# Kernel tuning notes

Measured on AMD Instinct MI355X. Metric: run time of the kernel, lower is better.

## Reference

```python
import jax, jax.numpy as jnp
import numpy as np

B, C, H_IMG, W_LEN = 32, 32, 16, 512
IN_CH = C * H_IMG          # 512, LSTM input size
OUT_CH = 1024              # bidirectional output size
HID = OUT_CH // 2          # 512, hidden per direction


def setup_inputs() -> dict:
    key = jax.random.key(0)
    ks = jax.random.split(key, 9)
    s = 1.0 / np.sqrt(HID)  # torch LSTM default init scale
    u = lambda k, shape: jax.random.uniform(k, shape, jnp.float32, -s, s)
    return {
        "x": jax.random.normal(ks[0], (B, C, H_IMG, W_LEN), jnp.float32),
        "W_ih_f": u(ks[1], (4 * HID, IN_CH)),
        "W_hh_f": u(ks[2], (4 * HID, HID)),
        "b_ih_f": u(ks[3], (4 * HID,)),
        "b_hh_f": u(ks[4], (4 * HID,)),
        "W_ih_b": u(ks[5], (4 * HID, IN_CH)),
        "W_hh_b": u(ks[6], (4 * HID, HID)),
        "b_ih_b": u(ks[7], (4 * HID,)),
        "b_hh_b": u(ks[8], (4 * HID,)),
    }


def _lstm_dir(x, W_ih, W_hh, b_ih, b_hh, reverse):
    # x: [B, T, IN] -> h sequence [B, T, HID]; torch gate order (i, f, g, o)
    xp = jnp.einsum('bti,gi->btg', x, W_ih) + b_ih + b_hh  # input proj for all steps
    xp = jnp.swapaxes(xp, 0, 1)  # [T, B, 4H]
    if reverse:
        xp = xp[::-1]
    h0 = jnp.zeros((x.shape[0], HID), x.dtype)

    def step(carry, xp_t):
        h, c = carry
        g = xp_t + h @ W_hh.T
        i, f, gg, o = jnp.split(g, 4, axis=-1)
        c = jax.nn.sigmoid(f) * c + jax.nn.sigmoid(i) * jnp.tanh(gg)
        h = jax.nn.sigmoid(o) * jnp.tanh(c)
        return (h, c), h

    _, hs = jax.lax.scan(step, (h0, h0), xp)  # hs: [T, B, HID]
    if reverse:
        hs = hs[::-1]
    return jnp.swapaxes(hs, 0, 1)  # [B, T, HID]


def reference(x, W_ih_f, W_hh_f, b_ih_f, b_hh_f, W_ih_b, W_hh_b, b_ih_b, b_hh_b):
    Bn, Cn, Hn, Wn = x.shape
    # permute(0,3,1,2).view(B, W, C*H): width is the time axis
    xs = jnp.transpose(x, (0, 3, 1, 2)).reshape(Bn, Wn, Cn * Hn)
    hf = _lstm_dir(xs, W_ih_f, W_hh_f, b_ih_f, b_hh_f, reverse=False)
    hb = _lstm_dir(xs, W_ih_b, W_hh_b, b_ih_b, b_hh_b, reverse=True)
    out = jnp.concatenate([hf, hb], axis=-1)        # [B, W, OUT]
    out = jnp.swapaxes(out, 1, 2)                    # [B, OUT, W]
    return out.reshape(Bn, -1, Hn, Wn)               # [B, OUT//H, H, W]
```

## Files before the change

kernel.cpp:

```cpp
#include <hip/hip_runtime.h>
#include <hip/hip_bf16.h>

#define BATCH 32
#define TLEN 512
#define INCH 512
#define HID 512

typedef __bf16 bf16x8 __attribute__((ext_vector_type(8)));
typedef float f32x4 __attribute__((ext_vector_type(4)));
using bf16 = __hip_bfloat16;

#define OFF_XS2   0ull
#define OFF_WCAT  16777216ull
#define OFF_WHHP  20971520ull
#define OFF_BIAS  25165824ull
#define OFF_HBUF  25182208ull
#define OFF_CTR   25313280ull
#define OFF_FLAG  25313536ull
#define OFF_XP    25321728ull
#define WS_REQUIRED (25321728ull + 134217728ull)

__device__ __forceinline__ float sigmoid_fast(float x) {
    return 1.f / (1.f + __expf(-x));
}
__device__ __forceinline__ float tanh_fast(float x) {
    float ax = fabsf(x);
    float e = __expf(-2.f * ax);
    float r = (1.f - e) / (1.f + e);
    return copysignf(r, x);
}

__global__ void ws_too_small_kernel(float* out) {
    if (threadIdx.x == 0 && blockIdx.x == 0) out[0] = 12345.0f;
}

__global__ void pack_x_kernel(const float* __restrict__ x, bf16* __restrict__ XS2) {
    int bx = blockIdx.x;
    int b  = bx >> 6;
    int tt = (bx >> 3) & 7;
    int kt = bx & 7;
    __shared__ float tile[64][65];
    int tid  = threadIdx.x;
    int row2 = tid >> 6;
    int col  = tid & 63;
#pragma unroll
    for (int i = 0; i < 16; ++i) {
        int row = i * 4 + row2;
        int k = kt * 64 + row;
        tile[row][col] = x[((b * 32 + (k >> 4)) * 16 + (k & 15)) * 512 + tt * 64 + col];
    }
    __syncthreads();
#pragma unroll
    for (int i = 0; i < 16; ++i) {
        int trow = i * 4 + row2;
        int t = tt * 64 + trow;
        XS2[(t * 32 + b) * 512 + kt * 64 + col] = __float2bfloat16(tile[col][trow]);
    }
}

__global__ void pack_w_kernel(const float* __restrict__ Wih_f, const float* __restrict__ Whh_f,
                              const float* __restrict__ bih_f, const float* __restrict__ bhh_f,
                              const float* __restrict__ Wih_b, const float* __restrict__ Whh_b,
                              const float* __restrict__ bih_b, const float* __restrict__ bhh_b,
                              bf16* __restrict__ Wcat, bf16* __restrict__ Whhp,
                              float* __restrict__ bias, unsigned int* __restrict__ hbuf32,
                              unsigned int* __restrict__ ctr, unsigned int* __restrict__ flags) {
    long idx = (long)blockIdx.x * 256 + threadIdx.x;
    if (idx < 262144) {
        long e = idx * 8;
        int m = (int)(e >> 9), k = (int)(e & 511);
        const float* src = (m < 2048) ? &Wih_f[(long)m * 512 + k]
                                      : &Wih_b[(long)(m - 2048) * 512 + k];
        bf16* dst = &Wcat[e];
#pragma unroll
        for (int j = 0; j < 8; ++j) dst[j] = __float2bfloat16(src[j]);
        return;
    }
    idx -= 262144;
    if (idx < 262144) {
        long e = idx * 8;
        int k  = (int)(e & 511);
        int lm = (int)((e >> 9) & 63);
        int s  = (int)((e >> 15) & 31);
        int dir = (int)(e >> 20);
        int grow = (lm >> 4) * 512 + s * 16 + (lm & 15);
        const float* W = dir ? Whh_b : Whh_f;
        const float* src = &W[(long)grow * 512 + k];
        bf16* dst = &Whhp[e];
#pragma unroll
        for (int j = 0; j < 8; ++j) dst[j] = __float2bfloat16(src[j]);
        return;
    }
    idx -= 262144;
    if (idx < 4096) {
        int dir = (int)(idx >> 11), g = (int)(idx & 2047);
        bias[idx] = (dir ? (bih_b[g] + bhh_b[g]) : (bih_f[g] + bhh_f[g]));
        return;
    }
    idx -= 4096;
    if (idx < 32768) { hbuf32[idx] = 0u; return; }
    idx -= 32768;
    if (idx < 64) { ctr[idx] = 0u; return; }
    idx -= 64;
    if (idx < 2048) { flags[idx] = 0u; return; }
}

__global__ __launch_bounds__(256, 2) void gemm_xp_kernel(const bf16* __restrict__ Wcat,
                                                         const bf16* __restrict__ XS2,
                                                         bf16* __restrict__ XP) {
    int bm = (blockIdx.x & 31) * 128;
    int bn = (blockIdx.x >> 5) * 128;
    __shared__ bf16 lA[128 * 40];
    __shared__ bf16 lB[128 * 40];
    int tid = threadIdx.x;
    int lane = tid & 63, w = tid >> 6;
    int wm = (w & 1) * 64, wn = (w >> 1) * 64;
    int fr = lane & 15, fq = lane >> 4;
    f32x4 acc[4][4] = {};
    int r = tid >> 2, c = tid & 3;
    for (int kt = 0; kt < 16; ++kt) {
        int k0 = kt * 32;
        *(bf16x8*)&lA[r * 40 + c * 8]        = *(const bf16x8*)&Wcat[(long)(bm + r) * 512 + k0 + c * 8];
        *(bf16x8*)&lA[(r + 64) * 40 + c * 8] = *(const bf16x8*)&Wcat[(long)(bm + r + 64) * 512 + k0 + c * 8];
        *(bf16x8*)&lB[r * 40 + c * 8]        = *(const bf16x8*)&XS2[(long)(bn + r) * 512 + k0 + c * 8];
        *(bf16x8*)&lB[(r + 64) * 40 + c * 8] = *(const bf16x8*)&XS2[(long)(bn + r + 64) * 512 + k0 + c * 8];
        __syncthreads();
        bf16x8 af[4], bfm[4];
#pragma unroll
        for (int i = 0; i < 4; ++i) af[i]  = *(const bf16x8*)&lA[(wm + i * 16 + fr) * 40 + fq * 8];
#pragma unroll
        for (int i = 0; i < 4; ++i) bfm[i] = *(const bf16x8*)&lB[(wn + i * 16 + fr) * 40 + fq * 8];
#pragma unroll
        for (int mi = 0; mi < 4; ++mi)
#pragma unroll
            for (int ni = 0; ni < 4; ++ni)
                acc[mi][ni] = __builtin_amdgcn_mfma_f32_16x16x32_bf16(af[mi], bfm[ni], acc[mi][ni], 0, 0, 0);
        __syncthreads();
    }
#pragma unroll
    for (int mi = 0; mi < 4; ++mi) {
#pragma unroll
        for (int rr = 0; rr < 4; ++rr) {
            int m = bm + wm + mi * 16 + fq * 4 + rr;
            int dir = m >> 11, cc = m & 2047;
            int gate = cc >> 9, u = cc & 511, s = u >> 4, ul = u & 15;
#pragma unroll
            for (int ni = 0; ni < 4; ++ni) {
                int n = bn + wn + ni * 16 + fr;
                int t = n >> 5, b = n & 31;
                long off = ((((long)(t * 2 + dir) * 32 + s) * 4 + gate) * 16 + ul) * 32 + b;
                XP[off] = __float2bfloat16(acc[mi][ni][rr]);
            }
        }
    }
}

__global__ __launch_bounds__(512, 2) void lstm_rec_kernel(const bf16* __restrict__ Whhp,
                                                          const bf16* __restrict__ XP,
                                                          const float* __restrict__ bias,
                                                          bf16* hbuf, float* out,
                                                          unsigned int* flags) {
    int bx = blockIdx.x;
    int dir = bx >> 5, s = bx & 31;
    int tid = threadIdx.x;
    int lane = tid & 63, w = tid >> 6;
    int mt = w & 3, nt = w >> 2;
    int fr = lane & 15, fq = lane >> 4;
    __shared__ float gbuf[64 * 32];
    __shared__ float obuf[16][512];
    __shared__ bf16  hstage[BATCH * 16];
    __shared__ bf16  hsh[32 * 520];

    const bf16* wbase = Whhp + ((long)((dir * 32 + s) * 64 + mt * 16 + fr)) * 512 + fq * 8;
    bf16x8 wA[16];
#pragma unroll
    for (int kt = 0; kt < 16; ++kt) wA[kt] = *(const bf16x8*)(wbase + kt * 32);

    int b = tid & 31, ul = (tid >> 5) & 15;
    float bias_i = bias[dir * 2048 + 0 * 512 + s * 16 + ul];
    float bias_f = bias[dir * 2048 + 1 * 512 + s * 16 + ul];
    float bias_g = bias[dir * 2048 + 2 * 512 + s * 16 + ul];
    float bias_o = bias[dir * 2048 + 3 * 512 + s * 16 + ul];
    float cstate = 0.f;
    bf16* hb_dir = hbuf + (long)dir * 2 * BATCH * HID;
    unsigned int* myflag = flags + bx * 32;
    const unsigned int* pollflag = flags + (dir * 32 + (lane & 31)) * 32;
    long orow = (long)b * 524288 + (long)(dir * 512 + s * 16 + ul) * 512;
    int srow = tid >> 4, scol = (tid & 15) * 32;
    int guard_budget = 1 << 21;

    for (int t = 0; t < TLEN; ++t) {
        int ttime = dir ? (TLEN - 1 - t) : t;
        const bf16* xpp = XP + (long)(ttime * 2 + dir) * 65536 + (long)s * 2048;
        float xi = __bfloat162float(xpp[(0 * 16 + ul) * 32 + b]);
        float xf = __bfloat162float(xpp[(1 * 16 + ul) * 32 + b]);
        float xg = __bfloat162float(xpp[(2 * 16 + ul) * 32 + b]);
        float xo = __bfloat162float(xpp[(3 * 16 + ul) * 32 + b]);

        if (t > 0) {
            unsigned int target = (unsigned int)t;
            for (;;) {
                unsigned int v = __hip_atomic_load(pollflag, __ATOMIC_RELAXED,
                                                   __HIP_MEMORY_SCOPE_AGENT);
                if (__all(v >= target)) break;
                if (--guard_budget <= 0) break;
            }
        }

        {
            const bf16* src = hb_dir + (long)(t & 1) * BATCH * HID + (long)srow * 512 + scol;
            f32x4 v0, v1, v2, v3;
            asm volatile(
                "global_load_dwordx4 %0, %4, off sc0 sc1\n\t"
                "global_load_dwordx4 %1, %4, off offset:16 sc0 sc1\n\t"
                "global_load_dwordx4 %2, %4, off offset:32 sc0 sc1\n\t"
                "global_load_dwordx4 %3, %4, off offset:48 sc0 sc1\n\t"
                "s_waitcnt vmcnt(0)"
                : "=v"(v0), "=v"(v1), "=v"(v2), "=v"(v3)
                : "v"(src) : "memory");
            bf16* d = &hsh[srow * 520 + scol];
            *(f32x4*)(d)      = v0;
            *(f32x4*)(d + 8)  = v1;
            *(f32x4*)(d + 16) = v2;
            *(f32x4*)(d + 24) = v3;
        }
        __syncthreads();

        f32x4 acc = {};
#pragma unroll
        for (int kt = 0; kt < 16; ++kt) {
            bf16x8 hB = *(const bf16x8*)&hsh[(nt * 16 + fr) * 520 + kt * 32 + fq * 8];
            acc = __builtin_amdgcn_mfma_f32_16x16x32_bf16(wA[kt], hB, acc, 0, 0, 0);
        }
#pragma unroll
        for (int rr = 0; rr < 4; ++rr)
            gbuf[(mt * 16 + fq * 4 + rr) * 32 + nt * 16 + fr] = acc[rr];
        __syncthreads();

        float gi = xi + bias_i + gbuf[(0 * 16 + ul) * 32 + b];
        float gf = xf + bias_f + gbuf[(1 * 16 + ul) * 32 + b];
        float gg = xg + bias_g + gbuf[(2 * 16 + ul) * 32 + b];
        float go = xo + bias_o + gbuf[(3 * 16 + ul) * 32 + b];
        float si = sigmoid_fast(gi), sf = sigmoid_fast(gf), so = sigmoid_fast(go);
        cstate = sf * cstate + si * tanh_fast(gg);
        float h = so * tanh_fast(cstate);

        hstage[b * 16 + ul] = __float2bfloat16(h);
        obuf[ttime & 15][tid] = h;
        __syncthreads();

        if (w == 0) {
            int hbb = lane >> 1, half = lane & 1;
            f32x4 hv = *(const f32x4*)&hstage[hbb * 16 + half * 8];
            bf16* dst = hb_dir + (long)((t + 1) & 1) * BATCH * HID + (long)hbb * 512
                        + s * 16 + half * 8;
            asm volatile("global_store_dwordx4 %0, %1, off sc0 sc1"
                         :: "v"(dst), "v"(hv) : "memory");
            asm volatile("s_waitcnt vmcnt(0)" ::: "memory");
            if (lane == 0)
                __hip_atomic_store(myflag, (unsigned int)(t + 1), __ATOMIC_RELAXED,
                                   __HIP_MEMORY_SCOPE_AGENT);
        }

        if ((t & 15) == 15) {
            int tb = ttime & ~15;
            float vals[16];
#pragma unroll
            for (int c = 0; c < 16; ++c) vals[c] = obuf[c][tid];
            float* op = out + orow + tb;
#pragma unroll
            for (int c4 = 0; c4 < 4; ++c4)
                *(f32x4*)(op + c4 * 4) = *(f32x4*)&vals[c4 * 4];
        }
    }
}

extern "C" void kernel_launch(void* const* d_in, const int* in_sizes, int n_in,
                              void* d_out, int out_size, void* d_ws, size_t ws_size,
                              hipStream_t stream) {
    const float* x     = (const float*)d_in[0];
    const float* Wih_f = (const float*)d_in[1];
    const float* Whh_f = (const float*)d_in[2];
    const float* bih_f = (const float*)d_in[3];
    const float* bhh_f = (const float*)d_in[4];
    const float* Wih_b = (const float*)d_in[5];
    const float* Whh_b = (const float*)d_in[6];
    const float* bih_b = (const float*)d_in[7];
    const float* bhh_b = (const float*)d_in[8];
    float* out = (float*)d_out;

    if (ws_size < WS_REQUIRED) {
        ws_too_small_kernel<<<1, 64, 0, stream>>>(out);
        return;
    }

    char* ws = (char*)d_ws;
    bf16* XS2  = (bf16*)(ws + OFF_XS2);
    bf16* Wcat = (bf16*)(ws + OFF_WCAT);
    bf16* Whhp = (bf16*)(ws + OFF_WHHP);
    float* bias = (float*)(ws + OFF_BIAS);
    bf16* hbuf = (bf16*)(ws + OFF_HBUF);
    unsigned int* ctr   = (unsigned int*)(ws + OFF_CTR);
    unsigned int* flags = (unsigned int*)(ws + OFF_FLAG);
    bf16* XP   = (bf16*)(ws + OFF_XP);

    pack_x_kernel<<<2048, 256, 0, stream>>>(x, XS2);
    pack_w_kernel<<<2201, 256, 0, stream>>>(Wih_f, Whh_f, bih_f, bhh_f,
                                            Wih_b, Whh_b, bih_b, bhh_b,
                                            Wcat, Whhp, bias, (unsigned int*)hbuf, ctr, flags);
    gemm_xp_kernel<<<4096, 256, 0, stream>>>(Wcat, XS2, XP);
    lstm_rec_kernel<<<64, 512, 0, stream>>>(Whhp, XP, bias, hbuf, out, flags);
}
```

Measured before the change: 2.037 ms.

## Remove LDS barriers from LSTM recurrence via gate-interleaved weights and per-wave flags

Reorders the W_hh packing, the bias and the XP layout so each MFMA output lane holds all four gates (i,f,g,o) of one unit and batch element. The cell update can then run straight from accumulator registers, with no shared-memory gate buffer. Each wave loads h directly from global memory into MFMA B operands, stores its own h values, and raises its own per-wave flag. Pollers read four flags with one dwordx4 load. This removes all three __syncthreads and the LDS staging per timestep, at the cost of finer-grained flag traffic, scattered 2-byte global stores, and redundant global h loads across waves.

```diff
diff --git a/kernel.cpp b/kernel.cpp
--- a/kernel.cpp
+++ b/kernel.cpp
@@ -8,6 +8,8 @@
 
 typedef __bf16 bf16x8 __attribute__((ext_vector_type(8)));
 typedef float f32x4 __attribute__((ext_vector_type(4)));
+typedef unsigned int u32x4 __attribute__((ext_vector_type(4)));
+typedef unsigned short u16x4 __attribute__((ext_vector_type(4)));
 using bf16 = __hip_bfloat16;
 
 #define OFF_XS2   0ull
@@ -28,6 +30,10 @@
     float e = __expf(-2.f * ax);
     float r = (1.f - e) / (1.f + e);
     return copysignf(r, x);
+}
+__device__ __forceinline__ float bf2f(unsigned short u) {
+    unsigned int i = ((unsigned int)u) << 16;
+    float f; __builtin_memcpy(&f, &i, 4); return f;
 }
 
 __global__ void ws_too_small_kernel(float* out) {
@@ -83,7 +89,7 @@
         int lm = (int)((e >> 9) & 63);
         int s  = (int)((e >> 15) & 31);
         int dir = (int)(e >> 20);
-        int grow = (lm >> 4) * 512 + s * 16 + (lm & 15);
+        int grow = (lm & 3) * 512 + s * 16 + (lm >> 2);
         const float* W = dir ? Whh_b : Whh_f;
         const float* src = &W[(long)grow * 512 + k];
         bf16* dst = &Whhp[e];
@@ -93,7 +99,10 @@
     }
     idx -= 262144;
     if (idx < 4096) {
-        int dir = (int)(idx >> 11), g = (int)(idx & 2047);
+        int dir  = (int)(idx >> 11);
+        int r    = (int)(idx & 2047);
+        int s    = r >> 6, ul = (r >> 2) & 15, gate = r & 3;
+        int g    = gate * 512 + s * 16 + ul;
         bias[idx] = (dir ? (bih_b[g] + bhh_b[g]) : (bih_f[g] + bhh_f[g]));
         return;
     }
@@ -148,7 +157,7 @@
             for (int ni = 0; ni < 4; ++ni) {
                 int n = bn + wn + ni * 16 + fr;
                 int t = n >> 5, b = n & 31;
-                long off = ((((long)(t * 2 + dir) * 32 + s) * 4 + gate) * 16 + ul) * 32 + b;
+                long off = ((long)(t * 2 + dir) * 32 + s) * 2048 + (long)(ul * 32 + b) * 4 + gate;
                 XP[off] = __float2bfloat16(acc[mi][ni][rr]);
             }
         }
@@ -166,108 +175,106 @@
     int lane = tid & 63, w = tid >> 6;
     int mt = w & 3, nt = w >> 2;
     int fr = lane & 15, fq = lane >> 4;
-    __shared__ float gbuf[64 * 32];
     __shared__ float obuf[16][512];
-    __shared__ bf16  hstage[BATCH * 16];
-    __shared__ bf16  hsh[32 * 520];
 
     const bf16* wbase = Whhp + ((long)((dir * 32 + s) * 64 + mt * 16 + fr)) * 512 + fq * 8;
     bf16x8 wA[16];
 #pragma unroll
     for (int kt = 0; kt < 16; ++kt) wA[kt] = *(const bf16x8*)(wbase + kt * 32);
 
-    int b = tid & 31, ul = (tid >> 5) & 15;
-    float bias_i = bias[dir * 2048 + 0 * 512 + s * 16 + ul];
-    float bias_f = bias[dir * 2048 + 1 * 512 + s * 16 + ul];
-    float bias_g = bias[dir * 2048 + 2 * 512 + s * 16 + ul];
-    float bias_o = bias[dir * 2048 + 3 * 512 + s * 16 + ul];
+    int ul = mt * 4 + fq;
+    int b  = nt * 16 + fr;
+    f32x4 bv = *(const f32x4*)&bias[((dir * 32 + s) * 16 + ul) * 4];
     float cstate = 0.f;
+
     bf16* hb_dir = hbuf + (long)dir * 2 * BATCH * HID;
-    unsigned int* myflag = flags + bx * 32;
-    const unsigned int* pollflag = flags + (dir * 32 + (lane & 31)) * 32;
-    long orow = (long)b * 524288 + (long)(dir * 512 + s * 16 + ul) * 512;
-    int srow = tid >> 4, scol = (tid & 15) * 32;
-    int guard_budget = 1 << 21;
+    unsigned int* myflag = flags + dir * 256 + s * 8 + w;
+    const unsigned int* pollptr = flags + dir * 256 + lane * 4;
+    bf16* hstore_base = hb_dir + (long)b * HID + s * 16 + ul;
+    const bf16* hload_base = hb_dir + (long)b * HID + fq * 8;
+    float* outrow = out + (long)b * 524288 + (long)(dir * 512 + s * 16 + ul) * 512;
+    int guard = 1 << 21;
 
     for (int t = 0; t < TLEN; ++t) {
         int ttime = dir ? (TLEN - 1 - t) : t;
-        const bf16* xpp = XP + (long)(ttime * 2 + dir) * 65536 + (long)s * 2048;
-        float xi = __bfloat162float(xpp[(0 * 16 + ul) * 32 + b]);
-        float xf = __bfloat162float(xpp[(1 * 16 + ul) * 32 + b]);
-        float xg = __bfloat162float(xpp[(2 * 16 + ul) * 32 + b]);
-        float xo = __bfloat162float(xpp[(3 * 16 + ul) * 32 + b]);
+        const bf16* xpp = XP + (long)(ttime * 2 + dir) * 65536 + s * 2048 + (ul * 32 + b) * 4;
+        u16x4 xv = *(const u16x4*)xpp;
 
         if (t > 0) {
-            unsigned int target = (unsigned int)t;
+            unsigned int tt = (unsigned int)t;
             for (;;) {
-                unsigned int v = __hip_atomic_load(pollflag, __ATOMIC_RELAXED,
-                                                   __HIP_MEMORY_SCOPE_AGENT);
-                if (__all(v >= target)) break;
-                if (--guard_budget <= 0) break;
+                u32x4 fv;
+                asm volatile("global_load_dwordx4 %0, %1, off sc0 sc1\n\t"
+                             "s_waitcnt vmcnt(0)"
+                             : "=&v"(fv) : "v"(pollptr) : "memory");
+                int ok = (fv.x >= tt) & (fv.y >= tt) & (fv.z >= tt) & (fv.w >= tt);
+                if (__all(ok)) break;
+                if (--guard <= 0) break;
             }
         }
 
-        {
-            const bf16* src = hb_dir + (long)(t & 1) * BATCH * HID + (long)srow * 512 + scol;
-            f32x4 v0, v1, v2, v3;
-            asm volatile(
-                "global_load_dwordx4 %0, %4, off sc0 sc1\n\t"
-                "global_load_dwordx4 %1, %4, off offset:16 sc0 sc1\n\t"
-                "global_load_dwordx4 %2, %4, off offset:32 sc0 sc1\n\t"
-                "global_load_dwordx4 %3, %4, off offset:48 sc0 sc1\n\t"
-                "s_waitcnt vmcnt(0)"
-                : "=v"(v0), "=v"(v1), "=v"(v2), "=v"(v3)
-                : "v"(src) : "memory");
-            bf16* d = &hsh[srow * 520 + scol];
-            *(f32x4*)(d)      = v0;
-            *(f32x4*)(d + 8)  = v1;
-            *(f32x4*)(d + 16) = v2;
-            *(f32x4*)(d + 24) = v3;
+        const bf16* hsrc = hload_base + (long)(t & 1) * (BATCH * HID);
+        bf16x8 hB[16];
+        asm volatile(
+            "global_load_dwordx4 %0, %8, off sc0 sc1\n\t"
+            "global_load_dwordx4 %1, %8, off offset:64 sc0 sc1\n\t"
+            "global_load_dwordx4 %2, %8, off offset:128 sc0 sc1\n\t"
+            "global_load_dwordx4 %3, %8, off offset:192 sc0 sc1\n\t"
+            "global_load_dwordx4 %4, %8, off offset:256 sc0 sc1\n\t"
+            "global_load_dwordx4 %5, %8, off offset:320 sc0 sc1\n\t"
+            "global_load_dwordx4 %6, %8, off offset:384 sc0 sc1\n\t"
+            "global_load_dwordx4 %7, %8, off offset:448 sc0 sc1"
+            : "=&v"(hB[0]), "=&v"(hB[1]), "=&v"(hB[2]), "=&v"(hB[3]),
+              "=&v"(hB[4]), "=&v"(hB[5]), "=&v"(hB[6]), "=&v"(hB[7])
+            : "v"(hsrc) : "memory");
+        asm volatile(
+            "global_load_dwordx4 %0, %8, off offset:512 sc0 sc1\n\t"
+            "global_load_dwordx4 %1, %8, off offset:576 sc0 sc1\n\t"
+            "global_load_dwordx4 %2, %8, off offset:640 sc0 sc1\n\t"
+            "global_load_dwordx4 %3, %8, off offset:704 sc0 sc1\n\t"
+            "global_load_dwordx4 %4, %8, off offset:768 sc0 sc1\n\t"
+            "global_load_dwordx4 %5, %8, off offset:832 sc0 sc1\n\t"
+            "global_load_dwordx4 %6, %8, off offset:896 sc0 sc1\n\t"
+            "global_load_dwordx4 %7, %8, off offset:960 sc0 sc1\n\t"
+            "s_waitcnt vmcnt(0)"
+            : "=&v"(hB[8]), "=&v"(hB[9]), "=&v"(hB[10]), "=&v"(hB[11]),
+              "=&v"(hB[12]), "=&v"(hB[13]), "=&v"(hB[14]), "=&v"(hB[15])
+            : "v"(hsrc) : "memory");
+        __builtin_amdgcn_sched_barrier(0);
+
+        f32x4 a0 = {}, a1 = {};
+#pragma unroll
+        for (int kt = 0; kt < 16; kt += 2) {
+            a0 = __builtin_amdgcn_mfma_f32_16x16x32_bf16(wA[kt],     hB[kt],     a0, 0, 0, 0);
+            a1 = __builtin_amdgcn_mfma_f32_16x16x32_bf16(wA[kt + 1], hB[kt + 1], a1, 0, 0, 0);
         }
-        __syncthreads();
-
-        f32x4 acc = {};
-#pragma unroll
-        for (int kt = 0; kt < 16; ++kt) {
-            bf16x8 hB = *(const bf16x8*)&hsh[(nt * 16 + fr) * 520 + kt * 32 + fq * 8];
-            acc = __builtin_amdgcn_mfma_f32_16x16x32_bf16(wA[kt], hB, acc, 0, 0, 0);
-        }
-#pragma unroll
-        for (int rr = 0; rr < 4; ++rr)
-            gbuf[(mt * 16 + fq * 4 + rr) * 32 + nt * 16 + fr] = acc[rr];
-        __syncthreads();
-
-        float gi = xi + bias_i + gbuf[(0 * 16 + ul) * 32 + b];
-        float gf = xf + bias_f + gbuf[(1 * 16 + ul) * 32 + b];
-        float gg = xg + bias_g + gbuf[(2 * 16 + ul) * 32 + b];
-        float go = xo + bias_o + gbuf[(3 * 16 + ul) * 32 + b];
+
+        float gi = a0[0] + a1[0] + bv[0] + bf2f(xv.x);
+        float gf = a0[1] + a1[1] + bv[1] + bf2f(xv.y);
+        float gg = a0[2] + a1[2] + bv[2] + bf2f(xv.z);
+        float go = a0[3] + a1[3] + bv[3] + bf2f(xv.w);
         float si = sigmoid_fast(gi), sf = sigmoid_fast(gf), so = sigmoid_fast(go);
         cstate = sf * cstate + si * tanh_fast(gg);
         float h = so * tanh_fast(cstate);
 
-        hstage[b * 16 + ul] = __float2bfloat16(h);
+        bf16 hb16 = __float2bfloat16(h);
+        unsigned short hsb; __builtin_memcpy(&hsb, &hb16, 2);
+        unsigned int hreg = hsb;
+        bf16* haddr = hstore_base + (long)((t + 1) & 1) * (BATCH * HID);
+        asm volatile("global_store_short %0, %1, off sc0 sc1"
+                     :: "v"(haddr), "v"(hreg) : "memory");
+        asm volatile("s_waitcnt vmcnt(0)" ::: "memory");
+        if (lane == 0)
+            __hip_atomic_store(myflag, (unsigned int)(t + 1), __ATOMIC_RELAXED,
+                               __HIP_MEMORY_SCOPE_AGENT);
+
         obuf[ttime & 15][tid] = h;
-        __syncthreads();
-
-        if (w == 0) {
-            int hbb = lane >> 1, half = lane & 1;
-            f32x4 hv = *(const f32x4*)&hstage[hbb * 16 + half * 8];
-            bf16* dst = hb_dir + (long)((t + 1) & 1) * BATCH * HID + (long)hbb * 512
-                        + s * 16 + half * 8;
-            asm volatile("global_store_dwordx4 %0, %1, off sc0 sc1"
-                         :: "v"(dst), "v"(hv) : "memory");
-            asm volatile("s_waitcnt vmcnt(0)" ::: "memory");
-            if (lane == 0)
-                __hip_atomic_store(myflag, (unsigned int)(t + 1), __ATOMIC_RELAXED,
-                                   __HIP_MEMORY_SCOPE_AGENT);
-        }
-
         if ((t & 15) == 15) {
             int tb = ttime & ~15;
             float vals[16];
 #pragma unroll
             for (int c = 0; c < 16; ++c) vals[c] = obuf[c][tid];
-            float* op = out + orow + tb;
+            float* op = outrow + tb;
 #pragma unroll
             for (int c4 = 0; c4 < 4; ++c4)
                 *(f32x4*)(op + c4 * 4) = *(f32x4*)&vals[c4 * 4];
```

Result: slower. 5.213 ms (+155.9%).

## Interleave gate rows so MFMA output lanes hold all four gates in registers

Applied to the files above, without the earlier changes.

Reorders the packed recurrent weights, bias and precomputed input projection so that each MFMA accumulator lane holds the i/f/g/o gates for one (unit, batch) pair. This removes the LDS gate buffer round trip and one block-wide barrier per timestep, and loads the four input-projection values with a single vector load. The MFMA chain is also split into four independent accumulators to shorten the dependency chain. The obuf index by tid may no longer match the new unit/batch mapping per thread, which risks wrong output ordering.

```diff
diff --git a/kernel.cpp b/kernel.cpp
--- a/kernel.cpp
+++ b/kernel.cpp
@@ -8,6 +8,7 @@
 
 typedef __bf16 bf16x8 __attribute__((ext_vector_type(8)));
 typedef float f32x4 __attribute__((ext_vector_type(4)));
+typedef unsigned short u16x4 __attribute__((ext_vector_type(4)));
 using bf16 = __hip_bfloat16;
 
 #define OFF_XS2   0ull
@@ -28,6 +29,10 @@
     float e = __expf(-2.f * ax);
     float r = (1.f - e) / (1.f + e);
     return copysignf(r, x);
+}
+__device__ __forceinline__ float bf2f(unsigned short u) {
+    unsigned int i = ((unsigned int)u) << 16;
+    float f; __builtin_memcpy(&f, &i, 4); return f;
 }
 
 __global__ void ws_too_small_kernel(float* out) {
@@ -83,7 +88,7 @@
         int lm = (int)((e >> 9) & 63);
         int s  = (int)((e >> 15) & 31);
         int dir = (int)(e >> 20);
-        int grow = (lm >> 4) * 512 + s * 16 + (lm & 15);
+        int grow = (lm & 3) * 512 + s * 16 + (lm >> 2);
         const float* W = dir ? Whh_b : Whh_f;
         const float* src = &W[(long)grow * 512 + k];
         bf16* dst = &Whhp[e];
@@ -93,7 +98,10 @@
     }
     idx -= 262144;
     if (idx < 4096) {
-        int dir = (int)(idx >> 11), g = (int)(idx & 2047);
+        int dir  = (int)(idx >> 11);
+        int r    = (int)(idx & 2047);
+        int s    = r >> 6, ul = (r >> 2) & 15, gate = r & 3;
+        int g    = gate * 512 + s * 16 + ul;
         bias[idx] = (dir ? (bih_b[g] + bhh_b[g]) : (bih_f[g] + bhh_f[g]));
         return;
     }
@@ -148,7 +156,7 @@
             for (int ni = 0; ni < 4; ++ni) {
                 int n = bn + wn + ni * 16 + fr;
                 int t = n >> 5, b = n & 31;
-                long off = ((((long)(t * 2 + dir) * 32 + s) * 4 + gate) * 16 + ul) * 32 + b;
+                long off = ((long)(t * 2 + dir) * 32 + s) * 2048 + (long)(ul * 32 + b) * 4 + gate;
                 XP[off] = __float2bfloat16(acc[mi][ni][rr]);
             }
         }
@@ -166,7 +174,6 @@
     int lane = tid & 63, w = tid >> 6;
     int mt = w & 3, nt = w >> 2;
     int fr = lane & 15, fq = lane >> 4;
-    __shared__ float gbuf[64 * 32];
     __shared__ float obuf[16][512];
     __shared__ bf16  hstage[BATCH * 16];
     __shared__ bf16  hsh[32 * 520];
@@ -176,26 +183,22 @@
 #pragma unroll
     for (int kt = 0; kt < 16; ++kt) wA[kt] = *(const bf16x8*)(wbase + kt * 32);
 
-    int b = tid & 31, ul = (tid >> 5) & 15;
-    float bias_i = bias[dir * 2048 + 0 * 512 + s * 16 + ul];
-    float bias_f = bias[dir * 2048 + 1 * 512 + s * 16 + ul];
-    float bias_g = bias[dir * 2048 + 2 * 512 + s * 16 + ul];
-    float bias_o = bias[dir * 2048 + 3 * 512 + s * 16 + ul];
+    int ul = mt * 4 + fq;
+    int b  = nt * 16 + fr;
+    f32x4 bv = *(const f32x4*)&bias[((dir * 32 + s) * 16 + ul) * 4];
     float cstate = 0.f;
+
     bf16* hb_dir = hbuf + (long)dir * 2 * BATCH * HID;
-    unsigned int* myflag = flags + bx * 32;
+    unsigned int* myflag = flags + (dir * 32 + s) * 32;
     const unsigned int* pollflag = flags + (dir * 32 + (lane & 31)) * 32;
-    long orow = (long)b * 524288 + (long)(dir * 512 + s * 16 + ul) * 512;
+    float* outrow = out + (long)b * 524288 + (long)(dir * 512 + s * 16 + ul) * 512;
     int srow = tid >> 4, scol = (tid & 15) * 32;
-    int guard_budget = 1 << 21;
+    int guard = 1 << 21;
 
     for (int t = 0; t < TLEN; ++t) {
         int ttime = dir ? (TLEN - 1 - t) : t;
-        const bf16* xpp = XP + (long)(ttime * 2 + dir) * 65536 + (long)s * 2048;
-        float xi = __bfloat162float(xpp[(0 * 16 + ul) * 32 + b]);
-        float xf = __bfloat162float(xpp[(1 * 16 + ul) * 32 + b]);
-        float xg = __bfloat162float(xpp[(2 * 16 + ul) * 32 + b]);
-        float xo = __bfloat162float(xpp[(3 * 16 + ul) * 32 + b]);
+        const bf16* xpp = XP + (long)(ttime * 2 + dir) * 65536 + s * 2048 + (ul * 32 + b) * 4;
+        u16x4 xv = *(const u16x4*)xpp;
 
         if (t > 0) {
             unsigned int target = (unsigned int)t;
@@ -203,7 +206,7 @@
                 unsigned int v = __hip_atomic_load(pollflag, __ATOMIC_RELAXED,
                                                    __HIP_MEMORY_SCOPE_AGENT);
                 if (__all(v >= target)) break;
-                if (--guard_budget <= 0) break;
+                if (--guard <= 0) break;
             }
         }
 
@@ -216,7 +219,7 @@
                 "global_load_dwordx4 %2, %4, off offset:32 sc0 sc1\n\t"
                 "global_load_dwordx4 %3, %4, off offset:48 sc0 sc1\n\t"
                 "s_waitcnt vmcnt(0)"
-                : "=v"(v0), "=v"(v1), "=v"(v2), "=v"(v3)
+                : "=&v"(v0), "=&v"(v1), "=&v"(v2), "=&v"(v3)
                 : "v"(src) : "memory");
             bf16* d = &hsh[srow * 520 + scol];
             *(f32x4*)(d)      = v0;
@@ -226,21 +229,24 @@
         }
         __syncthreads();
 
-        f32x4 acc = {};
-#pragma unroll
-        for (int kt = 0; kt < 16; ++kt) {
-            bf16x8 hB = *(const bf16x8*)&hsh[(nt * 16 + fr) * 520 + kt * 32 + fq * 8];
-            acc = __builtin_amdgcn_mfma_f32_16x16x32_bf16(wA[kt], hB, acc, 0, 0, 0);
-        }
-#pragma unroll
-        for (int rr = 0; rr < 4; ++rr)
-            gbuf[(mt * 16 + fq * 4 + rr) * 32 + nt * 16 + fr] = acc[rr];
-        __syncthreads();
-
-        float gi = xi + bias_i + gbuf[(0 * 16 + ul) * 32 + b];
-        float gf = xf + bias_f + gbuf[(1 * 16 + ul) * 32 + b];
-        float gg = xg + bias_g + gbuf[(2 * 16 + ul) * 32 + b];
-        float go = xo + bias_o + gbuf[(3 * 16 + ul) * 32 + b];
+        f32x4 a0 = {}, a1 = {}, a2 = {}, a3 = {};
+        const bf16* hrow = &hsh[(nt * 16 + fr) * 520 + fq * 8];
+#pragma unroll
+        for (int kt = 0; kt < 16; kt += 4) {
+            bf16x8 h0 = *(const bf16x8*)(hrow + (kt + 0) * 32);
+            bf16x8 h1 = *(const bf16x8*)(hrow + (kt + 1) * 32);
+            bf16x8 h2 = *(const bf16x8*)(hrow + (kt + 2) * 32);
+            bf16x8 h3 = *(const bf16x8*)(hrow + (kt + 3) * 32);
+            a0 = __builtin_amdgcn_mfma_f32_16x16x32_bf16(wA[kt + 0], h0, a0, 0, 0, 0);
+            a1 = __builtin_amdgcn_mfma_f32_16x16x32_bf16(wA[kt + 1], h1, a1, 0, 0, 0);
+            a2 = __builtin_amdgcn_mfma_f32_16x16x32_bf16(wA[kt + 2], h2, a2, 0, 0, 0);
+            a3 = __builtin_amdgcn_mfma_f32_16x16x32_bf16(wA[kt + 3], h3, a3, 0, 0, 0);
+        }
+
+        float gi = (a0[0] + a1[0]) + (a2[0] + a3[0]) + bv[0] + bf2f(xv.x);
+        float gf = (a0[1] + a1[1]) + (a2[1] + a3[1]) + bv[1] + bf2f(xv.y);
+        float gg = (a0[2] + a1[2]) + (a2[2] + a3[2]) + bv[2] + bf2f(xv.z);
+        float go = (a0[3] + a1[3]) + (a2[3] + a3[3]) + bv[3] + bf2f(xv.w);
         float si = sigmoid_fast(gi), sf = sigmoid_fast(gf), so = sigmoid_fast(go);
         cstate = sf * cstate + si * tanh_fast(gg);
         float h = so * tanh_fast(cstate);
@@ -267,7 +273,7 @@
             float vals[16];
 #pragma unroll
             for (int c = 0; c < 16; ++c) vals[c] = obuf[c][tid];
-            float* op = out + orow + tb;
+            float* op = outrow + tb;
 #pragma unroll
             for (int c4 = 0; c4 < 4; ++c4)
                 *(f32x4*)(op + c4 * 4) = *(f32x4*)&vals[c4 * 4];
```

Result: no change. 2.026 ms (-0.6%).
